# Kernel optimization log

Hardware: AMD Instinct MI355X
Metric: run time of the kernel (lower is better)

The kernel has to match this reference:

```python
import jax, jax.numpy as jnp
import numpy as np


def _lstm_layer(x, Wx, Wh, b):
    """Standard LSTM over time. x: [B,T,D], Wx/Wh: [D,4D], b: [4D]. Returns [B,T,D]."""
    B, T, D = x.shape
    # Precompute input contributions for all timesteps (one big GEMM).
    xg = jnp.einsum('btd,dg->btg', x, Wx) + b  # [B,T,4D]

    def step(carry, xg_t):
        h, c = carry
        g = xg_t + h @ Wh  # [B,4D]
        i, f, gg, o = jnp.split(g, 4, axis=-1)
        c = jax.nn.sigmoid(f) * c + jax.nn.sigmoid(i) * jnp.tanh(gg)
        h = jax.nn.sigmoid(o) * jnp.tanh(c)
        return (h, c), h

    h0 = jnp.zeros((B, D), x.dtype)
    c0 = jnp.zeros((B, D), x.dtype)
    (_, _), hs = jax.lax.scan(step, (h0, c0), jnp.swapaxes(xg, 0, 1))  # hs: [T,B,D]
    return jnp.swapaxes(hs, 0, 1)


def setup_inputs() -> dict:
    key = jax.random.key(0)
    ks = jax.random.split(key, 8)
    B, T, V, D = 4, 1024, 32000, 512
    s = 1.0 / np.sqrt(D)
    return {
        'tokens': jax.random.randint(ks[0], (B, T), 0, V, dtype=jnp.int32),
        'embed': jax.random.normal(ks[1], (V, D), jnp.float32),  # stddev=1.0 per embedding_init
        'Wx0': jax.random.normal(ks[2], (D, 4 * D), jnp.float32) * s,
        'Wh0': jax.random.normal(ks[3], (D, 4 * D), jnp.float32) * s,
        'b0': jnp.zeros((4 * D,), jnp.float32),
        'Wx1': jax.random.normal(ks[4], (D, 4 * D), jnp.float32) * s,
        'Wh1': jax.random.normal(ks[5], (D, 4 * D), jnp.float32) * s,
        'b1': jnp.zeros((4 * D,), jnp.float32),
        'Wout': jax.random.normal(ks[6], (D, V), jnp.float32) * s,
        'bout': jnp.zeros((V,), jnp.float32),
    }


def reference(tokens, embed, Wx0, Wh0, b0, Wx1, Wh1, b1, Wout, bout):
    # ShiftRight(axis=1): prepend 0 token, drop last.
    shifted = jnp.pad(tokens, ((0, 0), (1, 0)))[:, :-1]
    x = jnp.take(embed, shifted, axis=0)  # [B,T,D]
    x = _lstm_layer(x, Wx0, Wh0, b0)
    x = _lstm_layer(x, Wx1, Wh1, b1)
    # Dropout is deterministic=True -> identity.
    logits = jnp.einsum('btd,dv->btv', x, Wout) + bout  # [B,T,V]
    return logits
```

## Files before the change

### kernel.cpp

```cpp
#include <hip/hip_runtime.h>
#include <math.h>


#define TSEQ 1024
#define DIM  512
#define GDIM 2048
#define VOC  32000
#define SENT 0x7F7F7F7Fu

typedef unsigned uint4v __attribute__((ext_vector_type(4)));
typedef float    f4v    __attribute__((ext_vector_type(4)));
typedef short    short8 __attribute__((ext_vector_type(8)));
typedef float    f32x4  __attribute__((ext_vector_type(4)));

__device__ __forceinline__ uint4v poll_load16(const unsigned* p) {
    uint4v v;
    asm volatile("global_load_dwordx4 %0, %1, off sc1\n\t"
                 "s_waitcnt vmcnt(0)"
                 : "=v"(v) : "v"(p) : "memory");
    return v;
}
__device__ __forceinline__ void issue_load16(const unsigned* p, uint4v* v) {
    asm volatile("global_load_dwordx4 %0, %1, off sc1"
                 : "=&v"(*v) : "v"(p) : "memory");
}
__device__ __forceinline__ void wait_load16(uint4v* v) {
    asm volatile("s_waitcnt vmcnt(0)" : "+v"(*v) :: "memory");
}

__device__ __forceinline__ float fsig(float x) {
    return __builtin_amdgcn_rcpf(1.0f + __expf(-x));
}
__device__ __forceinline__ float ftanh_(float x) {
    return 1.0f - 2.0f * __builtin_amdgcn_rcpf(1.0f + __expf(2.0f * x));
}

__device__ __forceinline__ unsigned short f2bf(float x) {
    unsigned u = __builtin_bit_cast(unsigned, x);
    return (unsigned short)((u + 0x7FFFu + ((u >> 16) & 1u)) >> 16);
}
__device__ __forceinline__ float bf2f(unsigned short h) {
    return __builtin_bit_cast(float, (unsigned)h << 16);
}

__global__ void embed_kernel(const int* __restrict__ tokens,
                             const float* __restrict__ embed,
                             float* __restrict__ x)
{
    const int row = blockIdx.x;
    const int b = row >> 10;
    const int t = row & 1023;
    const int tok = (t == 0) ? 0 : tokens[b * TSEQ + t - 1];
    const float4* src = (const float4*)(embed + (size_t)tok * DIM);
    float4* dst = (float4*)(x + (size_t)row * DIM);
    dst[threadIdx.x] = src[threadIdx.x];
}

__global__ __launch_bounds__(256) void gemm_bias_f32(
    const float* __restrict__ A, const float* __restrict__ Bm,
    const float* __restrict__ bias, float* __restrict__ C,
    int M, int N, int K)
{
    constexpr int BK = 16;
    __shared__ float As[BK][128 + 4];
    __shared__ float Bs[BK][128 + 4];

    const int tid = threadIdx.x;
    const int m0 = blockIdx.y * 128;
    const int n0 = blockIdx.x * 128;
    const int tm = (tid >> 4) << 3;
    const int tn = (tid & 15) << 3;

    const int a_r = tid >> 2;
    const int a_c = (tid & 3) << 2;
    const int b_r = tid >> 5;
    const int b_c = (tid & 31) << 2;

    float acc[8][8] = {};

    for (int k0 = 0; k0 < K; k0 += BK) {
        const float4 av0 = *(const float4*)&A[(size_t)(m0 + a_r) * K + k0 + a_c];
        const float4 av1 = *(const float4*)&A[(size_t)(m0 + a_r + 64) * K + k0 + a_c];
        const float4 bv0 = *(const float4*)&Bm[(size_t)(k0 + b_r) * N + n0 + b_c];
        const float4 bv1 = *(const float4*)&Bm[(size_t)(k0 + b_r + 8) * N + n0 + b_c];
        __syncthreads();
        As[a_c + 0][a_r] = av0.x;  As[a_c + 1][a_r] = av0.y;
        As[a_c + 2][a_r] = av0.z;  As[a_c + 3][a_r] = av0.w;
        As[a_c + 0][a_r + 64] = av1.x;  As[a_c + 1][a_r + 64] = av1.y;
        As[a_c + 2][a_r + 64] = av1.z;  As[a_c + 3][a_r + 64] = av1.w;
        *(float4*)&Bs[b_r][b_c] = bv0;
        *(float4*)&Bs[b_r + 8][b_c] = bv1;
        __syncthreads();

        #pragma unroll
        for (int kk = 0; kk < BK; ++kk) {
            float a[8], bf[8];
            *(float4*)&a[0]  = *(const float4*)&As[kk][tm];
            *(float4*)&a[4]  = *(const float4*)&As[kk][tm + 4];
            *(float4*)&bf[0] = *(const float4*)&Bs[kk][tn];
            *(float4*)&bf[4] = *(const float4*)&Bs[kk][tn + 4];
            #pragma unroll
            for (int i = 0; i < 8; ++i)
                #pragma unroll
                for (int jx = 0; jx < 8; ++jx)
                    acc[i][jx] += a[i] * bf[jx];
        }
    }

    float bv[8];
    #pragma unroll
    for (int jx = 0; jx < 8; ++jx) bv[jx] = bias[n0 + tn + jx];

    #pragma unroll
    for (int i = 0; i < 8; ++i) {
        float* crow = C + (size_t)(m0 + tm + i) * N + (n0 + tn);
        float4 o0, o1;
        o0.x = acc[i][0] + bv[0]; o0.y = acc[i][1] + bv[1];
        o0.z = acc[i][2] + bv[2]; o0.w = acc[i][3] + bv[3];
        o1.x = acc[i][4] + bv[4]; o1.y = acc[i][5] + bv[5];
        o1.z = acc[i][6] + bv[6]; o1.w = acc[i][7] + bv[7];
        *(float4*)&crow[0] = o0;
        *(float4*)&crow[4] = o1;
    }
}

__global__ __launch_bounds__(512, 1) void lstm2_kernel(
    const float* __restrict__ xg1, const float* __restrict__ Wh0,
    const float* __restrict__ Wx1, const float* __restrict__ Wh1,
    const float* __restrict__ b1,
    float* __restrict__ h1c, float* __restrict__ h2c,
    float* __restrict__ hs2)
{
    const int layer = blockIdx.x >> 6;
    const int wg    = blockIdx.x & 63;
    const int tid   = threadIdx.x;
    const int dbase = wg * 8;
    const int j = tid & 31;
    const int s = tid >> 5;
    const int wcol = (j >> 3) * DIM + dbase + (j & 7);

    __shared__ f4v  hA[DIM];
    __shared__ f4v  hB[DIM];
    __shared__ float part[16][4][32];
    __shared__ float gate_lds[4][32];

    float wr[32], wx[32];
    {
        const float* Wrec = layer ? Wh1 : Wh0;
        #pragma unroll
        for (int r = 0; r < 32; ++r)
            wr[r] = Wrec[(size_t)(s * 32 + r) * GDIM + wcol];
        if (layer) {
            #pragma unroll
            for (int r = 0; r < 32; ++r)
                wx[r] = Wx1[(size_t)(s * 32 + r) * GDIM + wcol];
        }
    }
    float bias2 = 0.f;
    if (layer && tid < 128) bias2 = b1[wcol];

    float c_reg = 0.f;
    const unsigned* h1u = (const unsigned*)h1c;
    const unsigned* h2u = (const unsigned*)h2c;

    if (layer == 0) {
        for (int t = 0; t < TSEQ; ++t) {
            float xgv = 0.f;
            if (tid < 128) xgv = xg1[((size_t)s * TSEQ + t) * GDIM + wcol];

            if (t > 0) {
                const unsigned* p = h1u + ((size_t)(t - 1) * DIM + tid) * 4;
                uint4v u;
                do { u = poll_load16(p); }
                while (u.x == SENT || u.y == SENT || u.z == SENT || u.w == SENT);
                hA[tid] = __builtin_bit_cast(f4v, u);
            } else {
                hA[tid] = f4v{0.f, 0.f, 0.f, 0.f};
            }
            __syncthreads();

            float a0 = 0.f, a1 = 0.f, a2 = 0.f, a3 = 0.f;
            const f4v* hp = &hA[s * 32];
            #pragma unroll
            for (int r = 0; r < 32; ++r) {
                const f4v v = hp[r];
                a0 += v.x * wr[r]; a1 += v.y * wr[r];
                a2 += v.z * wr[r]; a3 += v.w * wr[r];
            }
            part[s][0][j] = a0; part[s][1][j] = a1;
            part[s][2][j] = a2; part[s][3][j] = a3;
            __syncthreads();

            if (tid < 128) {
                float sum = xgv;
                #pragma unroll
                for (int s2 = 0; s2 < 16; ++s2) sum += part[s2][s][j];
                gate_lds[s][j] = sum;
            }
            __syncthreads();

            if (tid < 32) {
                const int ub = tid >> 3, ud = tid & 7;
                const float iv = gate_lds[ub][ 0 + ud];
                const float fv = gate_lds[ub][ 8 + ud];
                const float gv = gate_lds[ub][16 + ud];
                const float ov = gate_lds[ub][24 + ud];
                const float ig = fsig(iv);
                const float fg = fsig(fv);
                const float og = fsig(ov);
                c_reg = fg * c_reg + ig * ftanh_(gv);
                const float hval = og * ftanh_(c_reg);
                __hip_atomic_store(&h1c[((size_t)t * DIM + dbase + ud) * 4 + ub],
                                   hval, __ATOMIC_RELAXED, __HIP_MEMORY_SCOPE_AGENT);
            }
        }
    } else {
        for (int t = 0; t < TSEQ; ++t) {
            const unsigned* p1 = h1u + ((size_t)t * DIM + tid) * 4;
            uint4v u1;
            issue_load16(p1, &u1);

            if (t > 0) {
                const unsigned* p = h2u + ((size_t)(t - 1) * DIM + tid) * 4;
                uint4v u;
                do { u = poll_load16(p); }
                while (u.x == SENT || u.y == SENT || u.z == SENT || u.w == SENT);
                hB[tid] = __builtin_bit_cast(f4v, u);
            } else {
                hB[tid] = f4v{0.f, 0.f, 0.f, 0.f};
            }
            __syncthreads();

            float a0 = 0.f, a1 = 0.f, a2 = 0.f, a3 = 0.f;
            {
                const f4v* hp = &hB[s * 32];
                #pragma unroll
                for (int r = 0; r < 32; ++r) {
                    const f4v v = hp[r];
                    a0 += v.x * wr[r]; a1 += v.y * wr[r];
                    a2 += v.z * wr[r]; a3 += v.w * wr[r];
                }
            }

            wait_load16(&u1);
            if (u1.x == SENT || u1.y == SENT || u1.z == SENT || u1.w == SENT) {
                do { u1 = poll_load16(p1); }
                while (u1.x == SENT || u1.y == SENT || u1.z == SENT || u1.w == SENT);
            }
            hA[tid] = __builtin_bit_cast(f4v, u1);
            __syncthreads();
            {
                const f4v* hp = &hA[s * 32];
                #pragma unroll
                for (int r = 0; r < 32; ++r) {
                    const f4v v = hp[r];
                    a0 += v.x * wx[r]; a1 += v.y * wx[r];
                    a2 += v.z * wx[r]; a3 += v.w * wx[r];
                }
            }
            part[s][0][j] = a0; part[s][1][j] = a1;
            part[s][2][j] = a2; part[s][3][j] = a3;
            __syncthreads();

            if (tid < 128) {
                float sum = bias2;
                #pragma unroll
                for (int s2 = 0; s2 < 16; ++s2) sum += part[s2][s][j];
                gate_lds[s][j] = sum;
            }
            __syncthreads();

            if (tid < 32) {
                const int ub = tid >> 3, ud = tid & 7;
                const float iv = gate_lds[ub][ 0 + ud];
                const float fv = gate_lds[ub][ 8 + ud];
                const float gv = gate_lds[ub][16 + ud];
                const float ov = gate_lds[ub][24 + ud];
                const float ig = fsig(iv);
                const float fg = fsig(fv);
                const float og = fsig(ov);
                c_reg = fg * c_reg + ig * ftanh_(gv);
                const float hval = og * ftanh_(c_reg);
                __hip_atomic_store(&h2c[((size_t)t * DIM + dbase + ud) * 4 + ub],
                                   hval, __ATOMIC_RELAXED, __HIP_MEMORY_SCOPE_AGENT);
                hs2[((size_t)ub * TSEQ + t) * DIM + dbase + ud] = hval;
            }
        }
    }
}

__global__ __launch_bounds__(256) void transpose_W(const float* __restrict__ W,
                                                   unsigned short* __restrict__ Wt)
{
    __shared__ float tile[32][256];
    const int tid = threadIdx.x;
    const int n0 = blockIdx.x * 256;
    const int k0 = blockIdx.y * 32;

    #pragma unroll 8
    for (int r = 0; r < 32; ++r)
        tile[r][tid] = W[(size_t)(k0 + r) * VOC + n0 + tid];
    __syncthreads();

    unsigned short pr[64];
    #pragma unroll
    for (int kk = 0; kk < 32; ++kk) {
        const float w = tile[kk][tid];
        const unsigned short h = f2bf(w);
        const unsigned short l = f2bf(w - bf2f(h));
        pr[2 * kk + 0] = h;
        pr[2 * kk + 1] = l;
    }
    unsigned short* dst = Wt + (size_t)(n0 + tid) * 1024 + 2 * k0;
    #pragma unroll
    for (int i = 0; i < 8; ++i)
        *(short8*)(dst + 8 * i) = *(short8*)&pr[8 * i];
}

__global__ __launch_bounds__(64) void convert_A(const float* __restrict__ A,
                                                unsigned short* __restrict__ At)
{
    const int row = blockIdx.x;
    const int tid = threadIdx.x;
    const float4 v0 = *(const float4*)&A[(size_t)row * DIM + tid * 8];
    const float4 v1 = *(const float4*)&A[(size_t)row * DIM + tid * 8 + 4];
    float vals[8] = {v0.x, v0.y, v0.z, v0.w, v1.x, v1.y, v1.z, v1.w};
    unsigned short pr[16];
    #pragma unroll
    for (int i = 0; i < 8; ++i) {
        const unsigned short h = f2bf(vals[i]);
        pr[2 * i + 0] = h;
        pr[2 * i + 1] = h;
    }
    unsigned short* dst = At + (size_t)row * 1024 + tid * 16;
    #pragma unroll
    for (int i = 0; i < 2; ++i)
        *(short8*)(dst + 8 * i) = *(short8*)&pr[8 * i];
}

__global__ __launch_bounds__(256) void mfma_logits(
    const unsigned short* __restrict__ Ab, const unsigned short* __restrict__ Wb,
    const float* __restrict__ bias, float* __restrict__ C)
{
    constexpr int KP = 1024, BK = 64, NKT = KP / BK;
    __shared__ unsigned short As[128 * 64];
    __shared__ unsigned short Bs[128 * 64];

    const int tid  = threadIdx.x;
    const int lane = tid & 63;
    const int w    = tid >> 6;
    const int wm   = w >> 1, wn = w & 1;
    const int m0 = blockIdx.y * 128;
    const int n0 = blockIdx.x * 128;

    const int srow = tid >> 1;
    const int s0   = (tid & 1) * 4;
    const unsigned short* gA = Ab + (size_t)(m0 + srow) * KP + s0 * 8;
    const unsigned short* gB = Wb + (size_t)(n0 + srow) * KP + s0 * 8;
    const int swz = srow & 7;

    f32x4 acc[4][4] = {};
    short8 ra[4], rb[4];

    #pragma unroll
    for (int c = 0; c < 4; ++c) {
        ra[c] = *(const short8*)(gA + c * 8);
        rb[c] = *(const short8*)(gB + c * 8);
    }

    #pragma unroll 1
    for (int kt = 0; kt < NKT; ++kt) {
        __syncthreads();
        #pragma unroll
        for (int c = 0; c < 4; ++c) {
            *(short8*)&As[srow * 64 + ((s0 + c) ^ swz) * 8] = ra[c];
            *(short8*)&Bs[srow * 64 + ((s0 + c) ^ swz) * 8] = rb[c];
        }
        __syncthreads();

        if (kt + 1 < NKT) {
            const int ko = (kt + 1) * BK;
            #pragma unroll
            for (int c = 0; c < 4; ++c) {
                ra[c] = *(const short8*)(gA + ko + c * 8);
                rb[c] = *(const short8*)(gB + ko + c * 8);
            }
        }

        #pragma unroll
        for (int kk = 0; kk < 2; ++kk) {
            const int q = kk * 4 + (lane >> 4);
            short8 a[4], b[4];
            #pragma unroll
            for (int i = 0; i < 4; ++i) {
                const int Ra = wm * 64 + i * 16 + (lane & 15);
                a[i] = *(const short8*)&As[Ra * 64 + (q ^ (Ra & 7)) * 8];
                const int Rb = wn * 64 + i * 16 + (lane & 15);
                b[i] = *(const short8*)&Bs[Rb * 64 + (q ^ (Rb & 7)) * 8];
            }
            #pragma unroll
            for (int i = 0; i < 4; ++i)
                #pragma unroll
                for (int jx = 0; jx < 4; ++jx)
                    acc[i][jx] = __builtin_amdgcn_mfma_f32_16x16x32_bf16(
                        a[i], b[jx], acc[i][jx], 0, 0, 0);
        }
    }

    float bv[4];
    #pragma unroll
    for (int jx = 0; jx < 4; ++jx)
        bv[jx] = bias[n0 + wn * 64 + jx * 16 + (lane & 15)];

    #pragma unroll
    for (int i = 0; i < 4; ++i) {
        #pragma unroll
        for (int jx = 0; jx < 4; ++jx) {
            const int col = n0 + wn * 64 + jx * 16 + (lane & 15);
            #pragma unroll
            for (int r = 0; r < 4; ++r) {
                const int row = m0 + wm * 64 + i * 16 + (lane >> 4) * 4 + r;
                C[(size_t)row * VOC + col] = acc[i][jx][r] + bv[jx];
            }
        }
    }
}

extern "C" void kernel_launch(void* const* d_in, const int* in_sizes, int n_in,
                              void* d_out, int out_size, void* d_ws, size_t ws_size,
                              hipStream_t stream)
{
    const int*   tokens = (const int*)d_in[0];
    const float* embed  = (const float*)d_in[1];
    const float* Wx0    = (const float*)d_in[2];
    const float* Wh0    = (const float*)d_in[3];
    const float* b0     = (const float*)d_in[4];
    const float* Wx1    = (const float*)d_in[5];
    const float* Wh1    = (const float*)d_in[6];
    const float* b1     = (const float*)d_in[7];
    const float* Wout   = (const float*)d_in[8];
    const float* bout   = (const float*)d_in[9];
    float* out = (float*)d_out;

    char* ws = (char*)d_ws;
    float* x   = (float*)(ws);
    float* xg1 = (float*)(ws + ((size_t)8u << 20));
    float* h1c = (float*)(ws + ((size_t)40u << 20));
    float* h2c = (float*)(ws + ((size_t)48u << 20));
    float* hs2 = x;
    unsigned short* At = (unsigned short*)(ws + ((size_t)56u << 20));
    unsigned short* Wt = (unsigned short*)(ws + ((size_t)64u << 20));

    const bool use_mfma = ws_size >= ((size_t)132u << 20);

    hipMemsetAsync(ws + ((size_t)40u << 20), 0x7F, (size_t)16u << 20, stream);

    embed_kernel<<<dim3(4096), dim3(128), 0, stream>>>(tokens, embed, x);
    gemm_bias_f32<<<dim3(16, 32), dim3(256), 0, stream>>>(x, Wx0, b0, xg1, 4096, 2048, 512);

    if (use_mfma)
        transpose_W<<<dim3(125, 16), dim3(256), 0, stream>>>(Wout, Wt);

    lstm2_kernel<<<dim3(128), dim3(512), 0, stream>>>(xg1, Wh0, Wx1, Wh1, b1, h1c, h2c, hs2);

    if (use_mfma) {
        convert_A<<<dim3(4096), dim3(64), 0, stream>>>(hs2, At);
        mfma_logits<<<dim3(250, 32), dim3(256), 0, stream>>>(At, Wt, bout, out);
    } else {
        gemm_bias_f32<<<dim3(250, 32), dim3(256), 0, stream>>>(hs2, Wout, bout, out, 4096, VOC, 512);
    }
}
```

Measured before the change: 3.318 ms.

## Use direct global-to-LDS loads with double-buffered tiles in logits GEMM

Replaces the register-staged global→LDS copy in the logits MFMA GEMM with global_load_lds direct-to-LDS transfers into a double-buffered shared tile. The next K tile is prefetched into the alternate buffer while the current one is consumed, synchronised with vmcnt waits and raw s_barriers. This aims to remove VGPR staging and ds_write traffic and to overlap loads with MFMA work. The cost is twice the LDS footprint, which may lower occupancy, and relying on manual waitcnt for correctness.

```diff
diff --git a/kernel.cpp b/kernel.cpp
--- a/kernel.cpp
+++ b/kernel.cpp
@@ -26,6 +26,12 @@
 }
 __device__ __forceinline__ void wait_load16(uint4v* v) {
     asm volatile("s_waitcnt vmcnt(0)" : "+v"(*v) :: "memory");
+}
+
+__device__ __forceinline__ void gload_lds16(const unsigned short* g, unsigned short* l) {
+    __builtin_amdgcn_global_load_lds(
+        (const __attribute__((address_space(1))) void*)(g),
+        (__attribute__((address_space(3))) void*)(l), 16, 0, 0);
 }
 
 __device__ __forceinline__ float fsig(float x) {
@@ -343,8 +349,8 @@
     const float* __restrict__ bias, float* __restrict__ C)
 {
     constexpr int KP = 1024, BK = 64, NKT = KP / BK;
-    __shared__ unsigned short As[128 * 64];
-    __shared__ unsigned short Bs[128 * 64];
+    __shared__ unsigned short As[2][128 * 64];
+    __shared__ unsigned short Bs[2][128 * 64];
 
     const int tid  = threadIdx.x;
     const int lane = tid & 63;
@@ -353,39 +359,36 @@
     const int m0 = blockIdx.y * 128;
     const int n0 = blockIdx.x * 128;
 
-    const int srow = tid >> 1;
-    const int s0   = (tid & 1) * 4;
-    const unsigned short* gA = Ab + (size_t)(m0 + srow) * KP + s0 * 8;
-    const unsigned short* gB = Wb + (size_t)(n0 + srow) * KP + s0 * 8;
-    const int swz = srow & 7;
+    const int r8    = lane >> 3;
+    const int gslot = (lane & 7) ^ r8;
+    const size_t arow = (size_t)(m0 + w * 32 + r8);
+    const size_t brow = (size_t)(n0 + w * 32 + r8);
 
     f32x4 acc[4][4] = {};
-    short8 ra[4], rb[4];
-
-    #pragma unroll
-    for (int c = 0; c < 4; ++c) {
-        ra[c] = *(const short8*)(gA + c * 8);
-        rb[c] = *(const short8*)(gB + c * 8);
+    int cur = 0;
+
+    #pragma unroll
+    for (int i = 0; i < 4; ++i) {
+        gload_lds16(Ab + (arow + i * 8) * KP + gslot * 8, &As[0][(w * 32 + i * 8) * 64]);
+        gload_lds16(Wb + (brow + i * 8) * KP + gslot * 8, &Bs[0][(w * 32 + i * 8) * 64]);
     }
 
     #pragma unroll 1
     for (int kt = 0; kt < NKT; ++kt) {
-        __syncthreads();
-        #pragma unroll
-        for (int c = 0; c < 4; ++c) {
-            *(short8*)&As[srow * 64 + ((s0 + c) ^ swz) * 8] = ra[c];
-            *(short8*)&Bs[srow * 64 + ((s0 + c) ^ swz) * 8] = rb[c];
-        }
-        __syncthreads();
-
         if (kt + 1 < NKT) {
             const int ko = (kt + 1) * BK;
             #pragma unroll
-            for (int c = 0; c < 4; ++c) {
-                ra[c] = *(const short8*)(gA + ko + c * 8);
-                rb[c] = *(const short8*)(gB + ko + c * 8);
-            }
-        }
+            for (int i = 0; i < 4; ++i) {
+                gload_lds16(Ab + (arow + i * 8) * KP + ko + gslot * 8,
+                            &As[cur ^ 1][(w * 32 + i * 8) * 64]);
+                gload_lds16(Wb + (brow + i * 8) * KP + ko + gslot * 8,
+                            &Bs[cur ^ 1][(w * 32 + i * 8) * 64]);
+            }
+            asm volatile("s_waitcnt vmcnt(8)" ::: "memory");
+        } else {
+            asm volatile("s_waitcnt vmcnt(0)" ::: "memory");
+        }
+        __builtin_amdgcn_s_barrier();
 
         #pragma unroll
         for (int kk = 0; kk < 2; ++kk) {
@@ -394,9 +397,9 @@
             #pragma unroll
             for (int i = 0; i < 4; ++i) {
                 const int Ra = wm * 64 + i * 16 + (lane & 15);
-                a[i] = *(const short8*)&As[Ra * 64 + (q ^ (Ra & 7)) * 8];
+                a[i] = *(const short8*)&As[cur][Ra * 64 + (q ^ (Ra & 7)) * 8];
                 const int Rb = wn * 64 + i * 16 + (lane & 15);
-                b[i] = *(const short8*)&Bs[Rb * 64 + (q ^ (Rb & 7)) * 8];
+                b[i] = *(const short8*)&Bs[cur][Rb * 64 + (q ^ (Rb & 7)) * 8];
             }
             #pragma unroll
             for (int i = 0; i < 4; ++i)
@@ -405,6 +408,8 @@
                     acc[i][jx] = __builtin_amdgcn_mfma_f32_16x16x32_bf16(
                         a[i], b[jx], acc[i][jx], 0, 0, 0);
         }
+        __builtin_amdgcn_s_barrier();
+        cur ^= 1;
     }
 
     float bv[4];
```

Measured after the change: 3.331 ms. No clear change (+0.4%).
